# Kernel optimization log

Hardware: AMD Instinct MI355X
Metric: run time of the kernel (lower is better)

The kernel has to match this reference:

```python
import jax, jax.numpy as jnp
import numpy as np

N = 50000      # nodes
E = 800000     # edges (before self-loops)
IN = 256       # in_channels
OUT = 64       # out_channels per head
H = 4          # heads (layer 0)
LEAKY = 0.2    # PyG GATConv negative_slope default


def setup_inputs() -> dict:
    key = jax.random.key(0)
    ks = jax.random.split(key, 16)
    g = 0.1
    inp = {
        "x": jax.random.normal(ks[0], (N, IN), jnp.float32),
        "edge_index": jax.random.randint(ks[1], (2, E), 0, N, dtype=jnp.int32),
        # layer 0: in -> H*OUT, concat=True
        "W0": jax.random.normal(ks[2], (IN, H * OUT), jnp.float32) * g,
        "a_src0": jax.random.normal(ks[3], (H, OUT), jnp.float32) * g,
        "a_dst0": jax.random.normal(ks[4], (H, OUT), jnp.float32) * g,
        "b0": jnp.zeros((H * OUT,), jnp.float32),
        # layer 1: H*OUT -> OUT, heads=1, concat=False
        "W1": jax.random.normal(ks[5], (H * OUT, OUT), jnp.float32) * g,
        "a_src1": jax.random.normal(ks[6], (1, OUT), jnp.float32) * g,
        "a_dst1": jax.random.normal(ks[7], (1, OUT), jnp.float32) * g,
        "b1": jnp.zeros((OUT,), jnp.float32),
        # layer 2: H*OUT -> OUT (input is OUT from layer 1? no: layer1 outputs OUT)
        "W2": jax.random.normal(ks[8], (OUT, OUT), jnp.float32) * g,
        "a_src2": jax.random.normal(ks[9], (1, OUT), jnp.float32) * g,
        "a_dst2": jax.random.normal(ks[10], (1, OUT), jnp.float32) * g,
        "b2": jnp.zeros((OUT,), jnp.float32),
    }
    return inp


def _gat_layer(x, src, dst, W, a_s, a_d, b, heads, concat):
    """PyG GATConv: per-head linear, edge attention logits, segment softmax
    over incoming edges of each destination node, scatter-sum aggregate."""
    n = x.shape[0]
    h = (x @ W).reshape(n, heads, -1)                      # [N, H, C]
    al_s = (h * a_s).sum(-1)                               # [N, H]
    al_d = (h * a_d).sum(-1)                               # [N, H]
    e = jax.nn.leaky_relu(al_s[src] + al_d[dst], LEAKY)    # [E', H]
    m = jax.ops.segment_max(e, dst, num_segments=n)        # [N, H]
    ex = jnp.exp(e - m[dst])
    den = jax.ops.segment_sum(ex, dst, num_segments=n)     # [N, H]
    alpha = ex / (den[dst] + 1e-16)                        # [E', H]
    out = jax.ops.segment_sum(alpha[:, :, None] * h[src], dst, num_segments=n)  # [N,H,C]
    out = out.reshape(n, -1) if concat else out.mean(axis=1)
    return out + b


def reference(x, edge_index, W0, a_src0, a_dst0, b0, W1, a_src1, a_dst1, b1,
              W2, a_src2, a_dst2, b2):
    n = x.shape[0]
    loop = jnp.arange(n, dtype=edge_index.dtype)
    src = jnp.concatenate([edge_index[0], loop])   # PyG add_self_loops=True
    dst = jnp.concatenate([edge_index[1], loop])
    h = _gat_layer(x, src, dst, W0, a_src0, a_dst0, b0, H, True)
    h = jax.nn.elu(h)
    h = _gat_layer(h, src, dst, W1, a_src1, a_dst1, b1, 1, False)
    h = jax.nn.elu(h)
    h = _gat_layer(h, src, dst, W2, a_src2, a_dst2, b2, 1, False)
    h = jax.nn.elu(h)
    return h
```

## Files before the change

### kernel.cpp

```cpp
#include <hip/hip_runtime.h>
#include <hip/hip_bf16.h>


typedef unsigned short ushort_t;
typedef __attribute__((ext_vector_type(8))) short short8;
typedef __attribute__((ext_vector_type(4))) float f32x4;

__device__ __forceinline__ float elu_f(float x){ return x > 0.f ? x : expm1f(x); }
__device__ __forceinline__ float lrelu_f(float x){ return x > 0.f ? x : 0.2f * x; }
__device__ __forceinline__ ushort_t f2b(float f){
  union { float f; unsigned u; } v; v.f = f;
  unsigned r = v.u + 0x7fff + ((v.u >> 16) & 1);
  return (ushort_t)(r >> 16);
}
__device__ __forceinline__ float b2f_lo(unsigned v){
  union { unsigned u; float f; } c; c.u = v << 16; return c.f;
}
__device__ __forceinline__ float b2f_hi(unsigned v){
  union { unsigned u; float f; } c; c.u = v & 0xffff0000u; return c.f;
}

__global__ __launch_bounds__(256) void prep_kernel(const int* __restrict__ ei,
                                                   int* __restrict__ cnt,
                                                   const float4* __restrict__ x4,
                                                   ushort4* __restrict__ xb4, int n4,
                                                   const float* __restrict__ W0,
                                                   ushort_t* __restrict__ W0p,
                                                   const float* __restrict__ W1,
                                                   ushort_t* __restrict__ W1p,
                                                   const float* __restrict__ W2,
                                                   ushort_t* __restrict__ W2p,
                                                   int E, int Etot, int eb, int fb){
  int bid = blockIdx.x; int t = threadIdx.x;
  if(bid < eb){
    int e = bid * 256 + t;
    if(e < Etot){
      int d = (e < E) ? ei[E + e] : (e - E);
      atomicAdd(&cnt[d], 1);
    }
  } else if(bid < eb + fb){
    int i = (bid - eb) * 256 + t;
    if(i < n4){
      float4 v = x4[i];
      ushort4 o;
      o.x = f2b(v.x); o.y = f2b(v.y); o.z = f2b(v.z); o.w = f2b(v.w);
      xb4[i] = o;
    }
  } else {
    int r = bid - eb - fb;
    if(r < 256){
      int i = r * 256 + t; int k = i >> 8, n = i & 255;
      W0p[(size_t)n * 256 + k] = f2b(W0[i]);
    } else if(r < 320){
      int i = (r - 256) * 256 + t; int k = i >> 6, n = i & 63;
      W1p[(size_t)n * 256 + k] = f2b(W1[i]);
    } else {
      int i = (r - 320) * 256 + t; int k = i >> 6, n = i & 63;
      W2p[(size_t)n * 64 + k] = f2b(W2[i]);
    }
  }
}

__global__ __launch_bounds__(256) void blocksum_kernel(const int* __restrict__ cnt,
                                                       int* __restrict__ bsum, int N){
  __shared__ int sm[256];
  int t = threadIdx.x;
  int i = blockIdx.x * 256 + t;
  sm[t] = (i < N) ? cnt[i] : 0;
  __syncthreads();
  for(int off = 128; off > 0; off >>= 1){
    if(t < off) sm[t] += sm[t + off];
    __syncthreads();
  }
  if(t == 0) bsum[blockIdx.x] = sm[0];
}

__global__ __launch_bounds__(256) void scan2_kernel(const int* __restrict__ cnt,
                                                    const int* __restrict__ bsum,
                                                    int* __restrict__ rowptr,
                                                    int* __restrict__ cursor,
                                                    int N, int Etot, int nb){
  __shared__ int sm[256];
  __shared__ int spfx;
  int t = threadIdx.x;
  int c = blockIdx.x;
  sm[t] = (t < c && t < nb) ? bsum[t] : 0;
  __syncthreads();
  for(int off = 128; off > 0; off >>= 1){
    if(t < off) sm[t] += sm[t + off];
    __syncthreads();
  }
  if(t == 0) spfx = sm[0];
  __syncthreads();
  int pfx = spfx;
  __syncthreads();
  int i = c * 256 + t;
  int v = (i < N) ? cnt[i] : 0;
  sm[t] = v;
  __syncthreads();
  for(int off = 1; off < 256; off <<= 1){
    int x = 0;
    if(t >= off) x = sm[t - off];
    __syncthreads();
    sm[t] += x;
    __syncthreads();
  }
  if(i < N){
    int ex = sm[t] - v + pfx;
    rowptr[i] = ex;
    cursor[i] = ex;
    if(i == N - 1) rowptr[N] = Etot;
  }
}

__global__ __launch_bounds__(256) void scatter_kernel(const int* __restrict__ ei,
                                                      int* __restrict__ cursor,
                                                      int* __restrict__ esrc,
                                                      int E, int Etot){
  int e = blockIdx.x * 256 + threadIdx.x;
  if(e >= Etot) return;
  int s, d;
  if(e < E){ s = ei[e]; d = ei[E + e]; } else { s = e - E; d = s; }
  int pos = atomicAdd(&cursor[d], 1);
  esrc[pos] = s;
}

#define SKP 264
__global__ __launch_bounds__(256) void gemm0_kernel(const ushort_t* __restrict__ A,
                                                    const ushort_t* __restrict__ Bp,
                                                    ushort_t* __restrict__ h0b,
                                                    const float* __restrict__ asrc,
                                                    const float* __restrict__ adst,
                                                    float* __restrict__ als,
                                                    float* __restrict__ ald, int M){
  __shared__ ushort_t As[32 * SKP];
  int t = threadIdx.x;
  int row0 = blockIdx.x * 32;
  {
    int c = t;
    #pragma unroll
    for(int it = 0; it < 4; it++, c += 256){
      int r = c >> 5;
      int kc = (c & 31) << 3;
      int gr = row0 + r;
      short8 v = {};
      if(gr < M) v = *(const short8*)(A + (size_t)gr * 256 + kc);
      *(short8*)(As + r * SKP + kc) = v;
    }
  }
  __syncthreads();
  int wave = t >> 6, lane = t & 63;
  int m = lane & 15, q = lane >> 4;
  int colb = wave;
  const ushort_t* Bq = Bp + (size_t)(colb * 64 + m) * 256 + q * 8;
  const ushort_t* A0 = As + m * SKP + q * 8;
  const ushort_t* A1 = As + (16 + m) * SKP + q * 8;
  f32x4 acc[2][4] = {};
  for(int k0 = 0; k0 < 256; k0 += 32){
    short8 bv[4];
    #pragma unroll
    for(int j = 0; j < 4; j++) bv[j] = *(const short8*)(Bq + (size_t)j * 16 * 256 + k0);
    short8 a0 = *(const short8*)(A0 + k0);
    short8 a1 = *(const short8*)(A1 + k0);
    #pragma unroll
    for(int j = 0; j < 4; j++){
      acc[0][j] = __builtin_amdgcn_mfma_f32_16x16x32_bf16(a0, bv[j], acc[0][j], 0, 0, 0);
      acc[1][j] = __builtin_amdgcn_mfma_f32_16x16x32_bf16(a1, bv[j], acc[1][j], 0, 0, 0);
    }
  }
  #pragma unroll
  for(int rt = 0; rt < 2; rt++){
    #pragma unroll
    for(int j = 0; j < 4; j++){
      int col = colb * 64 + j * 16 + m;
      #pragma unroll
      for(int i = 0; i < 4; i++){
        int gr = row0 + rt * 16 + q * 4 + i;
        if(gr < M) h0b[(size_t)gr * 256 + col] = f2b(acc[rt][j][i]);
      }
    }
    float vs[4] = {0,0,0,0}, vd[4] = {0,0,0,0};
    #pragma unroll
    for(int j = 0; j < 4; j++){
      int col = colb * 64 + j * 16 + m;
      float a_s = asrc[col], a_d = adst[col];
      #pragma unroll
      for(int i = 0; i < 4; i++){
        vs[i] = fmaf(acc[rt][j][i], a_s, vs[i]);
        vd[i] = fmaf(acc[rt][j][i], a_d, vd[i]);
      }
    }
    #pragma unroll
    for(int off = 8; off > 0; off >>= 1){
      #pragma unroll
      for(int i = 0; i < 4; i++){
        vs[i] += __shfl_down(vs[i], off, 16);
        vd[i] += __shfl_down(vd[i], off, 16);
      }
    }
    if(m == 0){
      #pragma unroll
      for(int i = 0; i < 4; i++){
        int gr = row0 + rt * 16 + q * 4 + i;
        if(gr < M){
          als[(size_t)gr * 4 + colb] = vs[i];
          ald[(size_t)gr * 4 + colb] = vd[i];
        }
      }
    }
  }
}

__global__ __launch_bounds__(256, 8) void agg0_kernel(const int* __restrict__ rowptr,
                                                      const int* __restrict__ esrc,
                                                      const uint2* __restrict__ h0b2,
                                                      const float4* __restrict__ als4,
                                                      const float4* __restrict__ ald4,
                                                      const float4* __restrict__ b4,
                                                      uint2* __restrict__ out2, int N){
  int t = threadIdx.x;
  int lane = t & 63;
  int n = blockIdx.x * 4 + (t >> 6);
  if(n >= N) return;
  int h = lane >> 4;
  int beg = rowptr[n], end = rowptr[n + 1];
  float adh = ((const float*)(ald4 + n))[h];
  float4 acc = make_float4(0.f, 0.f, 0.f, 0.f);
  float den = 0.f;
  for(int c0 = beg; c0 < end; c0 += 16){
    int e = c0 + (lane & 15);
    int s = n; float w = 0.f;
    if(e < end){
      s = esrc[e];
      w = expf(lrelu_f(((const float*)(als4 + s))[h] + adh));
    }
    int rem = end - c0;
    if(rem > 16) rem = 16;
    #pragma unroll
    for(int g = 0; g < 4; g++){
      if(g * 4 < rem){
        int si[4]; float wi[4]; uint2 v[4];
        #pragma unroll
        for(int ii = 0; ii < 4; ii++){
          int idx = (lane & 48) + g * 4 + ii;
          si[ii] = __shfl(s, idx, 64);
          wi[ii] = __shfl(w, idx, 64);
        }
        #pragma unroll
        for(int ii = 0; ii < 4; ii++)
          v[ii] = h0b2[((size_t)si[ii] << 6) + lane];
        #pragma unroll
        for(int ii = 0; ii < 4; ii++){
          acc.x = fmaf(wi[ii], b2f_lo(v[ii].x), acc.x);
          acc.y = fmaf(wi[ii], b2f_hi(v[ii].x), acc.y);
          acc.z = fmaf(wi[ii], b2f_lo(v[ii].y), acc.z);
          acc.w = fmaf(wi[ii], b2f_hi(v[ii].y), acc.w);
          den += wi[ii];
        }
      }
    }
  }
  float inv = 1.f / (den + 1e-16f);
  float4 bb = b4[lane];
  float v0 = elu_f(acc.x * inv + bb.x);
  float v1 = elu_f(acc.y * inv + bb.y);
  float v2 = elu_f(acc.z * inv + bb.z);
  float v3 = elu_f(acc.w * inv + bb.w);
  uint2 o;
  o.x = (unsigned)f2b(v0) | ((unsigned)f2b(v1) << 16);
  o.y = (unsigned)f2b(v2) | ((unsigned)f2b(v3) << 16);
  out2[((size_t)n << 6) + lane] = o;
}

__global__ __launch_bounds__(256) void mfma_gemm(const ushort_t* __restrict__ A,
                                                 const ushort_t* __restrict__ Bp,
                                                 ushort_t* __restrict__ Cp,
                                                 const float* __restrict__ asrc,
                                                 const float* __restrict__ adst,
                                                 float* __restrict__ als,
                                                 float* __restrict__ ald,
                                                 int M, int K, int NC){
  int wave = threadIdx.x >> 6;
  int lane = threadIdx.x & 63;
  int tile0 = (blockIdx.x * 4 + wave) * 2;
  if(tile0 * 16 >= M) return;
  bool two = (tile0 + 1) * 16 < M;
  int m = lane & 15, q = lane >> 4;
  const ushort_t* Ab = A + (size_t)(tile0 * 16 + m) * K + q * 8;
  const ushort_t* Bq = Bp + (size_t)m * K + q * 8;
  f32x4 acc[2][4] = {};
  for(int k0 = 0; k0 < K; k0 += 32){
    short8 bv[4];
    #pragma unroll
    for(int j = 0; j < 4; j++) bv[j] = *(const short8*)(Bq + (size_t)j * 16 * K + k0);
    short8 a0 = *(const short8*)(Ab + k0);
    #pragma unroll
    for(int j = 0; j < 4; j++)
      acc[0][j] = __builtin_amdgcn_mfma_f32_16x16x32_bf16(a0, bv[j], acc[0][j], 0, 0, 0);
    if(two){
      short8 a1 = *(const short8*)(Ab + (size_t)16 * K + k0);
      #pragma unroll
      for(int j = 0; j < 4; j++)
        acc[1][j] = __builtin_amdgcn_mfma_f32_16x16x32_bf16(a1, bv[j], acc[1][j], 0, 0, 0);
    }
  }
  #pragma unroll
  for(int r = 0; r < 2; r++){
    if(r == 1 && !two) break;
    int rowt = tile0 + r;
    #pragma unroll
    for(int j = 0; j < 4; j++){
      int col = j * 16 + m;
      #pragma unroll
      for(int i = 0; i < 4; i++){
        int rr = rowt * 16 + q * 4 + i;
        Cp[(size_t)rr * NC + col] = f2b(acc[r][j][i]);
      }
    }
    float vs[4] = {0,0,0,0}, vd[4] = {0,0,0,0};
    #pragma unroll
    for(int j = 0; j < 4; j++){
      int col = j * 16 + m;
      float a_s = asrc[col], a_d = adst[col];
      #pragma unroll
      for(int i = 0; i < 4; i++){
        vs[i] = fmaf(acc[r][j][i], a_s, vs[i]);
        vd[i] = fmaf(acc[r][j][i], a_d, vd[i]);
      }
    }
    #pragma unroll
    for(int off = 8; off > 0; off >>= 1){
      #pragma unroll
      for(int i = 0; i < 4; i++){
        vs[i] += __shfl_down(vs[i], off, 16);
        vd[i] += __shfl_down(vd[i], off, 16);
      }
    }
    if(m == 0){
      #pragma unroll
      for(int i = 0; i < 4; i++){
        int rr = rowt * 16 + q * 4 + i;
        als[rr] = vs[i];
        ald[rr] = vd[i];
      }
    }
  }
}

#define H2S 72
__global__ __launch_bounds__(256, 8) void agg1g2_kernel(const int* __restrict__ rowptr,
                                                        const int* __restrict__ esrc,
                                                        const uint2* __restrict__ g1b2,
                                                        const float* __restrict__ als1,
                                                        const float* __restrict__ ald1,
                                                        const float* __restrict__ b1,
                                                        const ushort_t* __restrict__ W2p,
                                                        const float* __restrict__ as2,
                                                        const float* __restrict__ ad2,
                                                        ushort_t* __restrict__ g2b,
                                                        float* __restrict__ als2,
                                                        float* __restrict__ ald2, int N){
  __shared__ ushort_t Hs[16 * H2S];
  __shared__ float aps[4][16], apd[4][16];
  int t = threadIdx.x;
  int wave = t >> 6, lane = t & 63;
  int nbase = blockIdx.x * 16;
  int g = lane >> 4;
  int p = lane & 15;
  int n = nbase + wave * 4 + g;
  int nl = wave * 4 + g;
  if(n < N){
    int beg = rowptr[n], end = rowptr[n + 1];
    float ad = ald1[n];
    float4 acc = make_float4(0.f, 0.f, 0.f, 0.f);
    float den = 0.f;
    for(int c0 = beg; c0 < end; c0 += 16){
      int e = c0 + p;
      int s = n; float w = 0.f;
      if(e < end){
        s = esrc[e];
        w = expf(lrelu_f(als1[s] + ad));
      }
      int rem = end - c0;
      if(rem > 16) rem = 16;
      #pragma unroll
      for(int gg = 0; gg < 4; gg++){
        if(gg * 4 < rem){
          #pragma unroll
          for(int ii = 0; ii < 4; ii++){
            int i = gg * 4 + ii;
            int idx = (lane & 48) + i;
            int si = __shfl(s, idx, 64);
            float wi = __shfl(w, idx, 64);
            uint2 v = g1b2[((size_t)si << 4) + p];
            acc.x = fmaf(wi, b2f_lo(v.x), acc.x);
            acc.y = fmaf(wi, b2f_hi(v.x), acc.y);
            acc.z = fmaf(wi, b2f_lo(v.y), acc.z);
            acc.w = fmaf(wi, b2f_hi(v.y), acc.w);
            den += wi;
          }
        }
      }
    }
    float inv = 1.f / (den + 1e-16f);
    float4 bb = ((const float4*)b1)[p];
    unsigned o0 = (unsigned)f2b(elu_f(acc.x * inv + bb.x)) |
                  ((unsigned)f2b(elu_f(acc.y * inv + bb.y)) << 16);
    unsigned o1 = (unsigned)f2b(elu_f(acc.z * inv + bb.z)) |
                  ((unsigned)f2b(elu_f(acc.w * inv + bb.w)) << 16);
    uint2 ov; ov.x = o0; ov.y = o1;
    *(uint2*)(Hs + nl * H2S + p * 4) = ov;
  }
  __syncthreads();
  int m = lane & 15, q = lane >> 4;
  const ushort_t* Bw = W2p + (size_t)(wave * 16 + m) * 64 + q * 8;
  const ushort_t* Aw = Hs + m * H2S + q * 8;
  f32x4 acc = {};
  #pragma unroll
  for(int k0 = 0; k0 < 64; k0 += 32){
    short8 av = *(const short8*)(Aw + k0);
    short8 bv = *(const short8*)(Bw + k0);
    acc = __builtin_amdgcn_mfma_f32_16x16x32_bf16(av, bv, acc, 0, 0, 0);
  }
  float a_s = as2[wave * 16 + m], a_d = ad2[wave * 16 + m];
  float vs[4], vd[4];
  #pragma unroll
  for(int i = 0; i < 4; i++){
    int gn = nbase + q * 4 + i;
    if(gn < N) g2b[(size_t)gn * 64 + wave * 16 + m] = f2b(acc[i]);
    vs[i] = acc[i] * a_s;
    vd[i] = acc[i] * a_d;
  }
  #pragma unroll
  for(int off = 8; off > 0; off >>= 1){
    #pragma unroll
    for(int i = 0; i < 4; i++){
      vs[i] += __shfl_down(vs[i], off, 16);
      vd[i] += __shfl_down(vd[i], off, 16);
    }
  }
  if(m == 0){
    #pragma unroll
    for(int i = 0; i < 4; i++){
      aps[wave][q * 4 + i] = vs[i];
      apd[wave][q * 4 + i] = vd[i];
    }
  }
  __syncthreads();
  if(t < 16){
    int gn = nbase + t;
    if(gn < N){
      als2[gn] = aps[0][t] + aps[1][t] + aps[2][t] + aps[3][t];
      ald2[gn] = apd[0][t] + apd[1][t] + apd[2][t] + apd[3][t];
    }
  }
}

__global__ __launch_bounds__(256, 8) void aggF_kernel(const int* __restrict__ rowptr,
                                                      const int* __restrict__ esrc,
                                                      const uint2* __restrict__ gb2,
                                                      const float* __restrict__ als,
                                                      const float* __restrict__ ald,
                                                      const float* __restrict__ b,
                                                      float4* __restrict__ outp, int N){
  int t = threadIdx.x;
  int lane = t & 63;
  int g = lane >> 4;
  int p = lane & 15;
  int n = blockIdx.x * 16 + (t >> 6) * 4 + g;
  if(n >= N) return;
  int beg = rowptr[n], end = rowptr[n + 1];
  float ad = ald[n];
  float4 acc = make_float4(0.f, 0.f, 0.f, 0.f);
  float den = 0.f;
  for(int c0 = beg; c0 < end; c0 += 16){
    int e = c0 + p;
    int s = n; float w = 0.f;
    if(e < end){
      s = esrc[e];
      w = expf(lrelu_f(als[s] + ad));
    }
    int rem = end - c0;
    if(rem > 16) rem = 16;
    #pragma unroll
    for(int gg = 0; gg < 4; gg++){
      if(gg * 4 < rem){
        #pragma unroll
        for(int ii = 0; ii < 4; ii++){
          int i = gg * 4 + ii;
          int idx = (lane & 48) + i;
          int si = __shfl(s, idx, 64);
          float wi = __shfl(w, idx, 64);
          uint2 v = gb2[((size_t)si << 4) + p];
          acc.x = fmaf(wi, b2f_lo(v.x), acc.x);
          acc.y = fmaf(wi, b2f_hi(v.x), acc.y);
          acc.z = fmaf(wi, b2f_lo(v.y), acc.z);
          acc.w = fmaf(wi, b2f_hi(v.y), acc.w);
          den += wi;
        }
      }
    }
  }
  float inv = 1.f / (den + 1e-16f);
  float4 bb = ((const float4*)b)[p];
  float4 o;
  o.x = elu_f(acc.x * inv + bb.x);
  o.y = elu_f(acc.y * inv + bb.y);
  o.z = elu_f(acc.z * inv + bb.z);
  o.w = elu_f(acc.w * inv + bb.w);
  outp[((size_t)n << 4) + p] = o;
}

extern "C" void kernel_launch(void* const* d_in, const int* in_sizes, int n_in,
                              void* d_out, int out_size, void* d_ws, size_t ws_size,
                              hipStream_t stream){
  const float* x   = (const float*)d_in[0];
  const int*   ei  = (const int*)d_in[1];
  const float* W0  = (const float*)d_in[2];
  const float* as0 = (const float*)d_in[3];
  const float* ad0 = (const float*)d_in[4];
  const float* b0  = (const float*)d_in[5];
  const float* W1  = (const float*)d_in[6];
  const float* as1 = (const float*)d_in[7];
  const float* ad1 = (const float*)d_in[8];
  const float* b1  = (const float*)d_in[9];
  const float* W2  = (const float*)d_in[10];
  const float* as2 = (const float*)d_in[11];
  const float* ad2 = (const float*)d_in[12];
  const float* b2  = (const float*)d_in[13];
  int N = in_sizes[0] / 256;
  int E = in_sizes[1] / 2;
  int Etot = E + N;

  size_t off = 0;
  auto alc = [&](size_t bytes) -> char* {
    char* p = (char*)d_ws + off;
    off += (bytes + 255) & ~(size_t)255;
    return p;
  };
  ushort_t* xb    = (ushort_t*)alc((size_t)N * 256 * 2);
  ushort_t* h0b   = (ushort_t*)alc((size_t)N * 256 * 2);
  float*    als   = (float*)alc((size_t)N * 4 * 4);
  float*    ald   = (float*)alc((size_t)N * 4 * 4);
  float*    als1  = (float*)alc((size_t)N * 4);
  float*    ald1  = (float*)alc((size_t)N * 4);
  float*    als2  = (float*)alc((size_t)N * 4);
  float*    ald2  = (float*)alc((size_t)N * 4);
  int*      esrc  = (int*)alc((size_t)Etot * 4);
  int*      rowptr= (int*)alc((size_t)(N + 1) * 4);
  int*      cnt   = (int*)alc((size_t)N * 4);
  int*      cursor= (int*)alc((size_t)N * 4);
  int*      bsum  = (int*)alc(256 * 4);
  ushort_t* W0p   = (ushort_t*)alc(256 * 256 * 2);
  ushort_t* W1p   = (ushort_t*)alc(256 * 64 * 2);
  ushort_t* W2p   = (ushort_t*)alc(64 * 64 * 2);

  ushort_t* h1b = xb;
  ushort_t* g1b = h0b;
  ushort_t* g2b = xb;

  int nb = (N + 255) / 256;
  int eb = (Etot + 255) / 256;
  int fb = (N * 64 + 255) / 256;
  int g0b = (N + 31) / 32;
  int rb = ((N / 16) + 7) / 8;
  int tb = (N + 15) / 16;
  int ab = (N + 3) / 4;
  int ab16 = (N + 15) / 16;

  hipMemsetAsync(cnt, 0, (size_t)N * 4, stream);
  prep_kernel<<<eb + fb + 336, 256, 0, stream>>>(ei, cnt, (const float4*)x,
                                                 (ushort4*)xb, N * 64,
                                                 W0, W0p, W1, W1p, W2, W2p,
                                                 E, Etot, eb, fb);
  blocksum_kernel<<<nb, 256, 0, stream>>>(cnt, bsum, N);
  scan2_kernel<<<nb, 256, 0, stream>>>(cnt, bsum, rowptr, cursor, N, Etot, nb);
  scatter_kernel<<<eb, 256, 0, stream>>>(ei, cursor, esrc, E, Etot);

  gemm0_kernel<<<g0b, 256, 0, stream>>>(xb, W0p, h0b, as0, ad0, als, ald, N);
  agg0_kernel<<<ab, 256, 0, stream>>>(rowptr, esrc, (const uint2*)h0b,
                                      (const float4*)als, (const float4*)ald,
                                      (const float4*)b0, (uint2*)h1b, N);

  mfma_gemm<<<rb, 256, 0, stream>>>(h1b, W1p, g1b, as1, ad1, als1, ald1,
                                    N, 256, 64);

  agg1g2_kernel<<<tb, 256, 0, stream>>>(rowptr, esrc, (const uint2*)g1b,
                                        als1, ald1, b1, W2p, as2, ad2,
                                        g2b, als2, ald2, N);

  aggF_kernel<<<ab16, 256, 0, stream>>>(rowptr, esrc, (const uint2*)g2b,
                                        als2, ald2, b2, (float4*)d_out, N);
}
```

Baseline: 366.3 us.

## Fuse layer-0 aggregation with layer-1 GEMM and attention logits

Merges the layer-0 aggregation kernel and the layer-1 MFMA GEMM into one kernel. Each block aggregates 4 nodes into shared memory as bf16, then runs a 16x16x32 MFMA against W1 and reduces the attention logits across waves. This removes the write and re-read of the intermediate N×256 bf16 activation and one kernel launch. In exchange, each block's MFMA uses only 4 of 16 rows (the rest are zero padding), every block re-reads W1, and two block barriers are added. Buffer aliasing for g1b and g2b is swapped to match.

```diff
diff --git a/kernel.cpp b/kernel.cpp
--- a/kernel.cpp
+++ b/kernel.cpp
@@ -211,138 +211,119 @@
   }
 }
 
-__global__ __launch_bounds__(256, 8) void agg0_kernel(const int* __restrict__ rowptr,
-                                                      const int* __restrict__ esrc,
-                                                      const uint2* __restrict__ h0b2,
-                                                      const float4* __restrict__ als4,
-                                                      const float4* __restrict__ ald4,
-                                                      const float4* __restrict__ b4,
-                                                      uint2* __restrict__ out2, int N){
+#define SKP2 264
+__global__ __launch_bounds__(256, 8) void agg0g1_kernel(const int* __restrict__ rowptr,
+                                                        const int* __restrict__ esrc,
+                                                        const uint2* __restrict__ h0b2,
+                                                        const float4* __restrict__ als4,
+                                                        const float4* __restrict__ ald4,
+                                                        const float4* __restrict__ b4,
+                                                        const ushort_t* __restrict__ W1p,
+                                                        const float* __restrict__ as1,
+                                                        const float* __restrict__ ad1,
+                                                        ushort_t* __restrict__ g1b,
+                                                        float* __restrict__ als1,
+                                                        float* __restrict__ ald1, int N){
+  __shared__ ushort_t Hs[4 * SKP2];
+  __shared__ float aps[4][4], apd[4][4];
   int t = threadIdx.x;
   int lane = t & 63;
-  int n = blockIdx.x * 4 + (t >> 6);
-  if(n >= N) return;
-  int h = lane >> 4;
-  int beg = rowptr[n], end = rowptr[n + 1];
-  float adh = ((const float*)(ald4 + n))[h];
-  float4 acc = make_float4(0.f, 0.f, 0.f, 0.f);
-  float den = 0.f;
-  for(int c0 = beg; c0 < end; c0 += 16){
-    int e = c0 + (lane & 15);
-    int s = n; float w = 0.f;
-    if(e < end){
-      s = esrc[e];
-      w = expf(lrelu_f(((const float*)(als4 + s))[h] + adh));
-    }
-    int rem = end - c0;
-    if(rem > 16) rem = 16;
-    #pragma unroll
-    for(int g = 0; g < 4; g++){
-      if(g * 4 < rem){
-        int si[4]; float wi[4]; uint2 v[4];
-        #pragma unroll
-        for(int ii = 0; ii < 4; ii++){
-          int idx = (lane & 48) + g * 4 + ii;
-          si[ii] = __shfl(s, idx, 64);
-          wi[ii] = __shfl(w, idx, 64);
+  int wave = t >> 6;
+  int nbase = blockIdx.x * 4;
+  int n = nbase + wave;
+  uint2 o; o.x = 0u; o.y = 0u;
+  if(n < N){
+    int h = lane >> 4;
+    int beg = rowptr[n], end = rowptr[n + 1];
+    float adh = ((const float*)(ald4 + n))[h];
+    float4 acc = make_float4(0.f, 0.f, 0.f, 0.f);
+    float den = 0.f;
+    for(int c0 = beg; c0 < end; c0 += 16){
+      int e = c0 + (lane & 15);
+      int s = n; float w = 0.f;
+      if(e < end){
+        s = esrc[e];
+        w = expf(lrelu_f(((const float*)(als4 + s))[h] + adh));
+      }
+      int rem = end - c0;
+      if(rem > 16) rem = 16;
+      #pragma unroll
+      for(int g = 0; g < 4; g++){
+        if(g * 4 < rem){
+          int si[4]; float wi[4]; uint2 v[4];
+          #pragma unroll
+          for(int ii = 0; ii < 4; ii++){
+            int idx = (lane & 48) + g * 4 + ii;
+            si[ii] = __shfl(s, idx, 64);
+            wi[ii] = __shfl(w, idx, 64);
+          }
+          #pragma unroll
+          for(int ii = 0; ii < 4; ii++)
+            v[ii] = h0b2[((size_t)si[ii] << 6) + lane];
+          #pragma unroll
+          for(int ii = 0; ii < 4; ii++){
+            acc.x = fmaf(wi[ii], b2f_lo(v[ii].x), acc.x);
+            acc.y = fmaf(wi[ii], b2f_hi(v[ii].x), acc.y);
+            acc.z = fmaf(wi[ii], b2f_lo(v[ii].y), acc.z);
+            acc.w = fmaf(wi[ii], b2f_hi(v[ii].y), acc.w);
+            den += wi[ii];
+          }
         }
-        #pragma unroll
-        for(int ii = 0; ii < 4; ii++)
-          v[ii] = h0b2[((size_t)si[ii] << 6) + lane];
-        #pragma unroll
-        for(int ii = 0; ii < 4; ii++){
-          acc.x = fmaf(wi[ii], b2f_lo(v[ii].x), acc.x);
-          acc.y = fmaf(wi[ii], b2f_hi(v[ii].x), acc.y);
-          acc.z = fmaf(wi[ii], b2f_lo(v[ii].y), acc.z);
-          acc.w = fmaf(wi[ii], b2f_hi(v[ii].y), acc.w);
-          den += wi[ii];
-        }
-      }
-    }
-  }
-  float inv = 1.f / (den + 1e-16f);
-  float4 bb = b4[lane];
-  float v0 = elu_f(acc.x * inv + bb.x);
-  float v1 = elu_f(acc.y * inv + bb.y);
-  float v2 = elu_f(acc.z * inv + bb.z);
-  float v3 = elu_f(acc.w * inv + bb.w);
-  uint2 o;
-  o.x = (unsigned)f2b(v0) | ((unsigned)f2b(v1) << 16);
-  o.y = (unsigned)f2b(v2) | ((unsigned)f2b(v3) << 16);
-  out2[((size_t)n << 6) + lane] = o;
-}
-
-__global__ __launch_bounds__(256) void mfma_gemm(const ushort_t* __restrict__ A,
-                                                 const ushort_t* __restrict__ Bp,
-                                                 ushort_t* __restrict__ Cp,
-                                                 const float* __restrict__ asrc,
-                                                 const float* __restrict__ adst,
-                                                 float* __restrict__ als,
-                                                 float* __restrict__ ald,
-                                                 int M, int K, int NC){
-  int wave = threadIdx.x >> 6;
-  int lane = threadIdx.x & 63;
-  int tile0 = (blockIdx.x * 4 + wave) * 2;
-  if(tile0 * 16 >= M) return;
-  bool two = (tile0 + 1) * 16 < M;
+      }
+    }
+    float inv = 1.f / (den + 1e-16f);
+    float4 bb = b4[lane];
+    float v0 = elu_f(acc.x * inv + bb.x);
+    float v1 = elu_f(acc.y * inv + bb.y);
+    float v2 = elu_f(acc.z * inv + bb.z);
+    float v3 = elu_f(acc.w * inv + bb.w);
+    o.x = (unsigned)f2b(v0) | ((unsigned)f2b(v1) << 16);
+    o.y = (unsigned)f2b(v2) | ((unsigned)f2b(v3) << 16);
+  }
+  *(uint2*)(Hs + wave * SKP2 + lane * 4) = o;
+  __syncthreads();
   int m = lane & 15, q = lane >> 4;
-  const ushort_t* Ab = A + (size_t)(tile0 * 16 + m) * K + q * 8;
-  const ushort_t* Bq = Bp + (size_t)m * K + q * 8;
-  f32x4 acc[2][4] = {};
-  for(int k0 = 0; k0 < K; k0 += 32){
-    short8 bv[4];
-    #pragma unroll
-    for(int j = 0; j < 4; j++) bv[j] = *(const short8*)(Bq + (size_t)j * 16 * K + k0);
-    short8 a0 = *(const short8*)(Ab + k0);
-    #pragma unroll
-    for(int j = 0; j < 4; j++)
-      acc[0][j] = __builtin_amdgcn_mfma_f32_16x16x32_bf16(a0, bv[j], acc[0][j], 0, 0, 0);
-    if(two){
-      short8 a1 = *(const short8*)(Ab + (size_t)16 * K + k0);
-      #pragma unroll
-      for(int j = 0; j < 4; j++)
-        acc[1][j] = __builtin_amdgcn_mfma_f32_16x16x32_bf16(a1, bv[j], acc[1][j], 0, 0, 0);
-    }
-  }
-  #pragma unroll
-  for(int r = 0; r < 2; r++){
-    if(r == 1 && !two) break;
-    int rowt = tile0 + r;
-    #pragma unroll
-    for(int j = 0; j < 4; j++){
-      int col = j * 16 + m;
-      #pragma unroll
-      for(int i = 0; i < 4; i++){
-        int rr = rowt * 16 + q * 4 + i;
-        Cp[(size_t)rr * NC + col] = f2b(acc[r][j][i]);
-      }
-    }
-    float vs[4] = {0,0,0,0}, vd[4] = {0,0,0,0};
-    #pragma unroll
-    for(int j = 0; j < 4; j++){
-      int col = j * 16 + m;
-      float a_s = asrc[col], a_d = adst[col];
-      #pragma unroll
-      for(int i = 0; i < 4; i++){
-        vs[i] = fmaf(acc[r][j][i], a_s, vs[i]);
-        vd[i] = fmaf(acc[r][j][i], a_d, vd[i]);
-      }
-    }
-    #pragma unroll
-    for(int off = 8; off > 0; off >>= 1){
-      #pragma unroll
-      for(int i = 0; i < 4; i++){
-        vs[i] += __shfl_down(vs[i], off, 16);
-        vd[i] += __shfl_down(vd[i], off, 16);
-      }
-    }
-    if(m == 0){
-      #pragma unroll
-      for(int i = 0; i < 4; i++){
-        int rr = rowt * 16 + q * 4 + i;
-        als[rr] = vs[i];
-        ald[rr] = vd[i];
-      }
+  const ushort_t* Bw = W1p + (size_t)(wave * 16 + m) * 256 + q * 8;
+  f32x4 acc1 = {};
+  #pragma unroll
+  for(int k0 = 0; k0 < 256; k0 += 32){
+    short8 av = {};
+    if(m < 4) av = *(const short8*)(Hs + m * SKP2 + q * 8 + k0);
+    short8 bv = *(const short8*)(Bw + k0);
+    acc1 = __builtin_amdgcn_mfma_f32_16x16x32_bf16(av, bv, acc1, 0, 0, 0);
+  }
+  if(q == 0){
+    #pragma unroll
+    for(int i = 0; i < 4; i++){
+      int gn = nbase + i;
+      if(gn < N) g1b[(size_t)gn * 64 + wave * 16 + m] = f2b(acc1[i]);
+    }
+  }
+  float a_s = as1[wave * 16 + m], a_d = ad1[wave * 16 + m];
+  float vs[4], vd[4];
+  #pragma unroll
+  for(int i = 0; i < 4; i++){
+    vs[i] = acc1[i] * a_s;
+    vd[i] = acc1[i] * a_d;
+  }
+  #pragma unroll
+  for(int off = 8; off > 0; off >>= 1){
+    #pragma unroll
+    for(int i = 0; i < 4; i++){
+      vs[i] += __shfl_down(vs[i], off, 16);
+      vd[i] += __shfl_down(vd[i], off, 16);
+    }
+  }
+  if(lane == 0){
+    #pragma unroll
+    for(int i = 0; i < 4; i++){ aps[wave][i] = vs[i]; apd[wave][i] = vd[i]; }
+  }
+  __syncthreads();
+  if(t < 4){
+    int gn = nbase + t;
+    if(gn < N){
+      als1[gn] = aps[0][t] + aps[1][t] + aps[2][t] + aps[3][t];
+      ald1[gn] = apd[0][t] + apd[1][t] + apd[2][t] + apd[3][t];
     }
   }
 }
@@ -555,15 +536,13 @@
   ushort_t* W1p   = (ushort_t*)alc(256 * 64 * 2);
   ushort_t* W2p   = (ushort_t*)alc(64 * 64 * 2);
 
-  ushort_t* h1b = xb;
-  ushort_t* g1b = h0b;
-  ushort_t* g2b = xb;
+  ushort_t* g1b = xb;
+  ushort_t* g2b = h0b;
 
   int nb = (N + 255) / 256;
   int eb = (Etot + 255) / 256;
   int fb = (N * 64 + 255) / 256;
   int g0b = (N + 31) / 32;
-  int rb = ((N / 16) + 7) / 8;
   int tb = (N + 15) / 16;
   int ab = (N + 3) / 4;
   int ab16 = (N + 15) / 16;
@@ -578,12 +557,11 @@
   scatter_kernel<<<eb, 256, 0, stream>>>(ei, cursor, esrc, E, Etot);
 
   gemm0_kernel<<<g0b, 256, 0, stream>>>(xb, W0p, h0b, as0, ad0, als, ald, N);
-  agg0_kernel<<<ab, 256, 0, stream>>>(rowptr, esrc, (const uint2*)h0b,
-                                      (const float4*)als, (const float4*)ald,
-                                      (const float4*)b0, (uint2*)h1b, N);
-
-  mfma_gemm<<<rb, 256, 0, stream>>>(h1b, W1p, g1b, as1, ad1, als1, ald1,
-                                    N, 256, 64);
+
+  agg0g1_kernel<<<ab, 256, 0, stream>>>(rowptr, esrc, (const uint2*)h0b,
+                                        (const float4*)als, (const float4*)ald,
+                                        (const float4*)b0, W1p, as1, ad1,
+                                        g1b, als1, ald1, N);
 
   agg1g2_kernel<<<tb, 256, 0, stream>>>(rowptr, esrc, (const uint2*)g1b,
                                         als1, ald1, b1, W2p, as2, ad2,
```

Result: slower. 380.3 us (+3.8%).

## Fuse x bf16 cast into gemm0 and slice h0 into column panels

Applied to the files above, without the earlier changes.

The fp32-to-bf16 conversion of x moves from the prep kernel into the gemm0 A-tile load, which removes one pass over x and the bf16 copy it writes. The layer-0 hidden features are now stored as 8 column slices of 32 features (slice-major). Each aggregation block handles one slice for 128 nodes, so the gathered rows touch a 16-wide working set per slice that should fit better in cache. gemm1 reads the sliced layout. The cost is more blocks, recomputation of the edge weights once per slice (8x the exp work), and narrower 64-byte gathers per node.

```diff
diff --git a/kernel.cpp b/kernel.cpp
--- a/kernel.cpp
+++ b/kernel.cpp
@@ -22,15 +22,13 @@
 
 __global__ __launch_bounds__(256) void prep_kernel(const int* __restrict__ ei,
                                                    int* __restrict__ cnt,
-                                                   const float4* __restrict__ x4,
-                                                   ushort4* __restrict__ xb4, int n4,
                                                    const float* __restrict__ W0,
                                                    ushort_t* __restrict__ W0p,
                                                    const float* __restrict__ W1,
                                                    ushort_t* __restrict__ W1p,
                                                    const float* __restrict__ W2,
                                                    ushort_t* __restrict__ W2p,
-                                                   int E, int Etot, int eb, int fb){
+                                                   int E, int Etot, int eb){
   int bid = blockIdx.x; int t = threadIdx.x;
   if(bid < eb){
     int e = bid * 256 + t;
@@ -38,16 +36,8 @@
       int d = (e < E) ? ei[E + e] : (e - E);
       atomicAdd(&cnt[d], 1);
     }
-  } else if(bid < eb + fb){
-    int i = (bid - eb) * 256 + t;
-    if(i < n4){
-      float4 v = x4[i];
-      ushort4 o;
-      o.x = f2b(v.x); o.y = f2b(v.y); o.z = f2b(v.z); o.w = f2b(v.w);
-      xb4[i] = o;
-    }
   } else {
-    int r = bid - eb - fb;
+    int r = bid - eb;
     if(r < 256){
       int i = r * 256 + t; int k = i >> 8, n = i & 255;
       W0p[(size_t)n * 256 + k] = f2b(W0[i]);
@@ -126,9 +116,9 @@
 }
 
 #define SKP 264
-__global__ __launch_bounds__(256) void gemm0_kernel(const ushort_t* __restrict__ A,
+__global__ __launch_bounds__(256) void gemm0_kernel(const float4* __restrict__ x4,
                                                     const ushort_t* __restrict__ Bp,
-                                                    ushort_t* __restrict__ h0b,
+                                                    ushort_t* __restrict__ h0s,
                                                     const float* __restrict__ asrc,
                                                     const float* __restrict__ adst,
                                                     float* __restrict__ als,
@@ -144,7 +134,14 @@
       int kc = (c & 31) << 3;
       int gr = row0 + r;
       short8 v = {};
-      if(gr < M) v = *(const short8*)(A + (size_t)gr * 256 + kc);
+      if(gr < M){
+        float4 f0 = x4[(size_t)gr * 64 + (kc >> 2)];
+        float4 f1 = x4[(size_t)gr * 64 + (kc >> 2) + 1];
+        v[0] = (short)f2b(f0.x); v[1] = (short)f2b(f0.y);
+        v[2] = (short)f2b(f0.z); v[3] = (short)f2b(f0.w);
+        v[4] = (short)f2b(f1.x); v[5] = (short)f2b(f1.y);
+        v[6] = (short)f2b(f1.z); v[7] = (short)f2b(f1.w);
+      }
       *(short8*)(As + r * SKP + kc) = v;
     }
   }
@@ -173,10 +170,11 @@
     #pragma unroll
     for(int j = 0; j < 4; j++){
       int col = colb * 64 + j * 16 + m;
+      size_t sbase = (size_t)(col >> 5) * M * 32;
       #pragma unroll
       for(int i = 0; i < 4; i++){
         int gr = row0 + rt * 16 + q * 4 + i;
-        if(gr < M) h0b[(size_t)gr * 256 + col] = f2b(acc[rt][j][i]);
+        if(gr < M) h0s[sbase + (size_t)gr * 32 + (col & 31)] = f2b(acc[rt][j][i]);
       }
     }
     float vs[4] = {0,0,0,0}, vd[4] = {0,0,0,0};
@@ -211,94 +209,94 @@
   }
 }
 
-__global__ __launch_bounds__(256, 8) void agg0_kernel(const int* __restrict__ rowptr,
+__global__ __launch_bounds__(256, 8) void aggs_kernel(const int* __restrict__ rowptr,
                                                       const int* __restrict__ esrc,
-                                                      const uint2* __restrict__ h0b2,
-                                                      const float4* __restrict__ als4,
-                                                      const float4* __restrict__ ald4,
-                                                      const float4* __restrict__ b4,
-                                                      uint2* __restrict__ out2, int N){
+                                                      const uint2* __restrict__ h0s,
+                                                      const float* __restrict__ als,
+                                                      const float* __restrict__ ald,
+                                                      const float* __restrict__ b0,
+                                                      uint2* __restrict__ h1s,
+                                                      int N){
   int t = threadIdx.x;
   int lane = t & 63;
-  int n = blockIdx.x * 4 + (t >> 6);
-  if(n >= N) return;
-  int h = lane >> 4;
-  int beg = rowptr[n], end = rowptr[n + 1];
-  float adh = ((const float*)(ald4 + n))[h];
-  float4 acc = make_float4(0.f, 0.f, 0.f, 0.f);
-  float den = 0.f;
-  for(int c0 = beg; c0 < end; c0 += 16){
-    int e = c0 + (lane & 15);
-    int s = n; float w = 0.f;
-    if(e < end){
-      s = esrc[e];
-      w = expf(lrelu_f(((const float*)(als4 + s))[h] + adh));
-    }
-    int rem = end - c0;
-    if(rem > 16) rem = 16;
-    #pragma unroll
-    for(int g = 0; g < 4; g++){
-      if(g * 4 < rem){
-        int si[4]; float wi[4]; uint2 v[4];
-        #pragma unroll
-        for(int ii = 0; ii < 4; ii++){
-          int idx = (lane & 48) + g * 4 + ii;
-          si[ii] = __shfl(s, idx, 64);
-          wi[ii] = __shfl(w, idx, 64);
+  int li = t & 7;
+  int p = blockIdx.x & 7;
+  int head = p >> 1;
+  int nbase = (blockIdx.x >> 3) * 128 + (t >> 3) * 4;
+  const uint2* Hp = h0s + (size_t)p * N * 8;
+  uint2* Op = h1s + (size_t)p * N * 8;
+  float4 bb = ((const float4*)b0)[p * 8 + li];
+  for(int j = 0; j < 4; j++){
+    int n = nbase + j;
+    if(n >= N) continue;
+    int beg = rowptr[n], end = rowptr[n + 1];
+    float adh = ald[(size_t)n * 4 + head];
+    float4 acc = make_float4(0.f, 0.f, 0.f, 0.f);
+    float den = 0.f;
+    for(int c0 = beg; c0 < end; c0 += 8){
+      int e = c0 + li;
+      int s = n; float w = 0.f;
+      if(e < end){
+        s = esrc[e];
+        w = expf(lrelu_f(als[(size_t)s * 4 + head] + adh));
+      }
+      int rem = end - c0;
+      if(rem > 8) rem = 8;
+      #pragma unroll
+      for(int g = 0; g < 2; g++){
+        if(g * 4 < rem){
+          #pragma unroll
+          for(int ii = 0; ii < 4; ii++){
+            int idx = (lane & 56) + g * 4 + ii;
+            int si = __shfl(s, idx, 64);
+            float wi = __shfl(w, idx, 64);
+            uint2 v = Hp[(size_t)si * 8 + li];
+            acc.x = fmaf(wi, b2f_lo(v.x), acc.x);
+            acc.y = fmaf(wi, b2f_hi(v.x), acc.y);
+            acc.z = fmaf(wi, b2f_lo(v.y), acc.z);
+            acc.w = fmaf(wi, b2f_hi(v.y), acc.w);
+            den += wi;
+          }
         }
-        #pragma unroll
-        for(int ii = 0; ii < 4; ii++)
-          v[ii] = h0b2[((size_t)si[ii] << 6) + lane];
-        #pragma unroll
-        for(int ii = 0; ii < 4; ii++){
-          acc.x = fmaf(wi[ii], b2f_lo(v[ii].x), acc.x);
-          acc.y = fmaf(wi[ii], b2f_hi(v[ii].x), acc.y);
-          acc.z = fmaf(wi[ii], b2f_lo(v[ii].y), acc.z);
-          acc.w = fmaf(wi[ii], b2f_hi(v[ii].y), acc.w);
-          den += wi[ii];
-        }
-      }
-    }
-  }
-  float inv = 1.f / (den + 1e-16f);
-  float4 bb = b4[lane];
-  float v0 = elu_f(acc.x * inv + bb.x);
-  float v1 = elu_f(acc.y * inv + bb.y);
-  float v2 = elu_f(acc.z * inv + bb.z);
-  float v3 = elu_f(acc.w * inv + bb.w);
-  uint2 o;
-  o.x = (unsigned)f2b(v0) | ((unsigned)f2b(v1) << 16);
-  o.y = (unsigned)f2b(v2) | ((unsigned)f2b(v3) << 16);
-  out2[((size_t)n << 6) + lane] = o;
-}
-
-__global__ __launch_bounds__(256) void mfma_gemm(const ushort_t* __restrict__ A,
-                                                 const ushort_t* __restrict__ Bp,
-                                                 ushort_t* __restrict__ Cp,
-                                                 const float* __restrict__ asrc,
-                                                 const float* __restrict__ adst,
-                                                 float* __restrict__ als,
-                                                 float* __restrict__ ald,
-                                                 int M, int K, int NC){
+      }
+    }
+    float inv = 1.f / (den + 1e-16f);
+    uint2 o;
+    o.x = (unsigned)f2b(elu_f(acc.x * inv + bb.x)) |
+          ((unsigned)f2b(elu_f(acc.y * inv + bb.y)) << 16);
+    o.y = (unsigned)f2b(elu_f(acc.z * inv + bb.z)) |
+          ((unsigned)f2b(elu_f(acc.w * inv + bb.w)) << 16);
+    Op[(size_t)n * 8 + li] = o;
+  }
+}
+
+__global__ __launch_bounds__(256) void gemm1_kernel(const ushort_t* __restrict__ h1s,
+                                                    const ushort_t* __restrict__ Bp,
+                                                    ushort_t* __restrict__ Cp,
+                                                    const float* __restrict__ asrc,
+                                                    const float* __restrict__ adst,
+                                                    float* __restrict__ als,
+                                                    float* __restrict__ ald, int M){
   int wave = threadIdx.x >> 6;
   int lane = threadIdx.x & 63;
   int tile0 = (blockIdx.x * 4 + wave) * 2;
   if(tile0 * 16 >= M) return;
   bool two = (tile0 + 1) * 16 < M;
   int m = lane & 15, q = lane >> 4;
-  const ushort_t* Ab = A + (size_t)(tile0 * 16 + m) * K + q * 8;
-  const ushort_t* Bq = Bp + (size_t)m * K + q * 8;
+  int r0 = tile0 * 16 + m;
+  const ushort_t* Bq = Bp + (size_t)m * 256 + q * 8;
   f32x4 acc[2][4] = {};
-  for(int k0 = 0; k0 < K; k0 += 32){
+  for(int k0 = 0; k0 < 256; k0 += 32){
+    const ushort_t* Hk = h1s + (size_t)(k0 >> 5) * M * 32 + q * 8;
     short8 bv[4];
     #pragma unroll
-    for(int j = 0; j < 4; j++) bv[j] = *(const short8*)(Bq + (size_t)j * 16 * K + k0);
-    short8 a0 = *(const short8*)(Ab + k0);
+    for(int j = 0; j < 4; j++) bv[j] = *(const short8*)(Bq + (size_t)j * 16 * 256 + k0);
+    short8 a0 = *(const short8*)(Hk + (size_t)r0 * 32);
     #pragma unroll
     for(int j = 0; j < 4; j++)
       acc[0][j] = __builtin_amdgcn_mfma_f32_16x16x32_bf16(a0, bv[j], acc[0][j], 0, 0, 0);
     if(two){
-      short8 a1 = *(const short8*)(Ab + (size_t)16 * K + k0);
+      short8 a1 = *(const short8*)(Hk + (size_t)(r0 + 16) * 32);
       #pragma unroll
       for(int j = 0; j < 4; j++)
         acc[1][j] = __builtin_amdgcn_mfma_f32_16x16x32_bf16(a1, bv[j], acc[1][j], 0, 0, 0);
@@ -314,7 +312,7 @@
       #pragma unroll
       for(int i = 0; i < 4; i++){
         int rr = rowt * 16 + q * 4 + i;
-        Cp[(size_t)rr * NC + col] = f2b(acc[r][j][i]);
+        Cp[(size_t)rr * 64 + col] = f2b(acc[r][j][i]);
       }
     }
     float vs[4] = {0,0,0,0}, vd[4] = {0,0,0,0};
@@ -538,8 +536,8 @@
     off += (bytes + 255) & ~(size_t)255;
     return p;
   };
-  ushort_t* xb    = (ushort_t*)alc((size_t)N * 256 * 2);
-  ushort_t* h0b   = (ushort_t*)alc((size_t)N * 256 * 2);
+  ushort_t* h0s   = (ushort_t*)alc((size_t)8 * N * 32 * 2);
+  ushort_t* h1s   = (ushort_t*)alc((size_t)8 * N * 32 * 2);
   float*    als   = (float*)alc((size_t)N * 4 * 4);
   float*    ald   = (float*)alc((size_t)N * 4 * 4);
   float*    als1  = (float*)alc((size_t)N * 4);
@@ -555,35 +553,31 @@
   ushort_t* W1p   = (ushort_t*)alc(256 * 64 * 2);
   ushort_t* W2p   = (ushort_t*)alc(64 * 64 * 2);
 
-  ushort_t* h1b = xb;
-  ushort_t* g1b = h0b;
-  ushort_t* g2b = xb;
+  ushort_t* g2b = h0s;
+  ushort_t* g1b = h0s + (size_t)4 * N * 32;
 
   int nb = (N + 255) / 256;
   int eb = (Etot + 255) / 256;
-  int fb = (N * 64 + 255) / 256;
   int g0b = (N + 31) / 32;
   int rb = ((N / 16) + 7) / 8;
   int tb = (N + 15) / 16;
-  int ab = (N + 3) / 4;
   int ab16 = (N + 15) / 16;
+  int asb = ((N + 127) / 128) * 8;
 
   hipMemsetAsync(cnt, 0, (size_t)N * 4, stream);
-  prep_kernel<<<eb + fb + 336, 256, 0, stream>>>(ei, cnt, (const float4*)x,
-                                                 (ushort4*)xb, N * 64,
-                                                 W0, W0p, W1, W1p, W2, W2p,
-                                                 E, Etot, eb, fb);
+  prep_kernel<<<eb + 336, 256, 0, stream>>>(ei, cnt, W0, W0p, W1, W1p, W2, W2p,
+                                            E, Etot, eb);
   blocksum_kernel<<<nb, 256, 0, stream>>>(cnt, bsum, N);
   scan2_kernel<<<nb, 256, 0, stream>>>(cnt, bsum, rowptr, cursor, N, Etot, nb);
   scatter_kernel<<<eb, 256, 0, stream>>>(ei, cursor, esrc, E, Etot);
 
-  gemm0_kernel<<<g0b, 256, 0, stream>>>(xb, W0p, h0b, as0, ad0, als, ald, N);
-  agg0_kernel<<<ab, 256, 0, stream>>>(rowptr, esrc, (const uint2*)h0b,
-                                      (const float4*)als, (const float4*)ald,
-                                      (const float4*)b0, (uint2*)h1b, N);
-
-  mfma_gemm<<<rb, 256, 0, stream>>>(h1b, W1p, g1b, as1, ad1, als1, ald1,
-                                    N, 256, 64);
+  gemm0_kernel<<<g0b, 256, 0, stream>>>((const float4*)x, W0p, h0s,
+                                        as0, ad0, als, ald, N);
+
+  aggs_kernel<<<asb, 256, 0, stream>>>(rowptr, esrc, (const uint2*)h0s,
+                                       als, ald, b0, (uint2*)h1s, N);
+
+  gemm1_kernel<<<rb, 256, 0, stream>>>(h1s, W1p, g1b, as1, ad1, als1, ald1, N);
 
   agg1g2_kernel<<<tb, 256, 0, stream>>>(rowptr, esrc, (const uint2*)g1b,
                                         als1, ald1, b1, W2p, as2, ad2,
```

New measurement: 393.0 us. 7.3% more time.
